# Optimization experiments

Hardware: AMD Instinct MI355X
Metric: run time of the kernel (lower is better)

The kernel has to match this reference:

```python
import jax, jax.numpy as jnp
from jax import lax
import numpy as np

THRESHOLD = 0.9
KHALF = 5  # conv_kernel_size; full conv width = 2*KHALF + 1 = 11


def _cif_scan(eouts, alpha_norm, elens, ylens, Lp1):
    """Vectorized-over-batch integrate-and-fire scan over time (lax.scan)."""
    B, T, D = eouts.shape
    bidx = jnp.arange(B)
    dt = eouts.dtype

    def step(carry, xs):
        alpha_accum, state, n_tok, fired = carry
        a_t, e_t, t = xs  # a_t: [B], e_t: [B,D], t: scalar int
        alpha_accum = alpha_accum + a_t
        active = (t <= elens - 1) & (n_tok < ylens)
        fire = active & (alpha_accum >= THRESHOLD)
        ak1 = 1.0 - alpha_accum
        ak2 = a_t - ak1
        # attention-weight column for time t
        aw_col = jnp.zeros((B, Lp1), dt)
        w_old = jnp.where(fire, ak1, jnp.where(active, a_t, jnp.zeros((), dt)))
        aw_col = aw_col.at[bidx, n_tok].add(w_old)
        n_new = n_tok + fire.astype(n_tok.dtype)
        aw_col = aw_col.at[bidx, n_new].add(jnp.where(fire, ak2, jnp.zeros((), dt)))
        # fired output row (set once per token slot)
        fire_val = state + ak1[:, None] * e_t
        cur = fired[bidx, n_tok]
        fired = fired.at[bidx, n_tok].set(jnp.where(fire[:, None], fire_val, cur))
        # integrate / reset state
        state = jnp.where(fire[:, None], ak2[:, None] * e_t,
                          jnp.where(active[:, None], state + a_t[:, None] * e_t, state))
        alpha_accum = jnp.where(fire, ak2, alpha_accum)
        return (alpha_accum, state, n_new, fired), aw_col

    init = (jnp.zeros((B,), dt), jnp.zeros((B, D), dt),
            jnp.zeros((B,), jnp.int32), jnp.zeros((B, Lp1, D), dt))
    xs = (jnp.swapaxes(alpha_norm, 0, 1), jnp.swapaxes(eouts, 0, 1),
          jnp.arange(T))
    (_, _, _, fired), aw_cols = lax.scan(step, init, xs)
    aws = jnp.transpose(aw_cols, (1, 2, 0))[:, None]  # [B,1,Lp1,T]
    return fired, aws


def _forward(eouts, conv_w, conv_b, proj_w, proj_b, elens, ylens, L):
    # Conv1d over time, 'same' padding: [B,T,D] -> [B,T,C]
    conv_feat = lax.conv_general_dilated(
        eouts, conv_w, window_strides=(1,), padding=[(KHALF, KHALF)],
        dimension_numbers=('NWC', 'WIO', 'NWC')) + conv_b
    alpha = jax.nn.sigmoid(conv_feat @ proj_w + proj_b)[:, :, 0]  # [B,T]
    alpha_norm = alpha / jnp.sum(alpha, axis=1, keepdims=True) \
        * ylens[:, None].astype(alpha.dtype)
    fired, aws = _cif_scan(eouts, alpha_norm, elens, ylens, L + 1)
    return fired[:, :L], alpha, aws


def setup_inputs():
    key = jax.random.key(0)
    k1, k2, k3, k4, k5 = jax.random.split(key, 5)
    B, T, D, C = 16, 2048, 512, 512
    eouts = jax.random.normal(k1, (B, T, D), jnp.float32)
    elens = jnp.maximum(jax.random.randint(k2, (B,), 0, T), T // 2).astype(jnp.int32)
    ylens = jnp.maximum(jax.random.randint(k3, (B,), 0, 128), 32).astype(jnp.int32)
    conv_w = jax.random.normal(k4, (2 * KHALF + 1, D, C), jnp.float32) * 0.02
    conv_b = jnp.zeros((C,), jnp.float32)
    proj_w = jax.random.normal(k5, (C, 1), jnp.float32) * 0.05
    proj_b = jnp.zeros((1,), jnp.float32)
    return dict(eouts=eouts, conv_w=conv_w, conv_b=conv_b,
                proj_w=proj_w, proj_b=proj_b, elens=elens, ylens=ylens)


def reference(eouts, conv_w, conv_b, proj_w, proj_b, elens, ylens):
    L = int(jnp.max(ylens))  # max_len = ylens.max(), as in the original
    return _forward(eouts, conv_w, conv_b, proj_w, proj_b, elens, ylens, L)
```

## Files before the change

### kernel.cpp

```cpp
#include <hip/hip_runtime.h>
#include <math.h>

#define KHALF 5
#define MAXF 256

__device__ inline float readlane_f(float v, int lane) {
    return __int_as_float(__builtin_amdgcn_readlane(__float_as_int(v), lane));
}

__global__ void k_prep(const float* __restrict__ conv_w, const float* __restrict__ conv_b,
                       const float* __restrict__ proj_w, const float* __restrict__ proj_b,
                       float* __restrict__ w_eff, float* __restrict__ b_eff,
                       int KD, int C,
                       float* __restrict__ aws, long long awsN, int WB, int NFILL) {
    if ((int)blockIdx.x >= WB) {
        long long N4 = awsN >> 2;
        long long gid = (long long)(blockIdx.x - WB) * 256 + threadIdx.x;
        float4 z = make_float4(0.f, 0.f, 0.f, 0.f);
        float4* a4 = reinterpret_cast<float4*>(aws);
        long long stride = (long long)NFILL * 256;
        for (long long i = gid; i < N4; i += stride) a4[i] = z;
        int tail = (int)(awsN & 3);
        if (gid < tail) aws[4 * N4 + gid] = 0.f;
        return;
    }
    int gid = blockIdx.x * blockDim.x + threadIdx.x;
    int wave = gid >> 6;
    int lane = gid & 63;
    if (wave > KD) return;
    float s = 0.f;
    if (wave < KD) {
        const float* row = conv_w + (size_t)wave * C;
        for (int c = lane * 4; c < C; c += 256) {
            float4 v = *reinterpret_cast<const float4*>(row + c);
            float4 w = *reinterpret_cast<const float4*>(proj_w + c);
            s += v.x * w.x + v.y * w.y + v.z * w.z + v.w * w.w;
        }
    } else {
        for (int c = lane; c < C; c += 64) s += conv_b[c] * proj_w[c];
    }
#pragma unroll
    for (int off = 32; off > 0; off >>= 1) s += __shfl_down(s, off, 64);
    if (lane == 0) {
        if (wave < KD) w_eff[wave] = s;
        else           b_eff[0] = s + proj_b[0];
    }
}

__global__ __launch_bounds__(256) void k_qdot(const float* __restrict__ eouts,
                                              const float* __restrict__ w_eff,
                                              float* __restrict__ q, int BT) {
    __shared__ float tile[64 * 68];
    __shared__ float wls[11 * 68];
    __shared__ float part[64 * 89];
    const int u0 = blockIdx.x * 64;
    const int rp = threadIdx.x & 31;
    const int s8 = threadIdx.x >> 5;
    float acc0[11], acc1[11];
#pragma unroll
    for (int k = 0; k < 11; ++k) { acc0[k] = 0.f; acc1[k] = 0.f; }

    float4 rv[4];
    float4 wv;
    auto issue = [&](int c) {
#pragma unroll
        for (int it = 0; it < 4; ++it) {
            int idx = it * 256 + threadIdx.x;
            int r = idx >> 4, j4 = idx & 15;
            rv[it] = *reinterpret_cast<const float4*>(
                eouts + (size_t)(u0 + r) * 512 + c * 64 + j4 * 4);
        }
        if (threadIdx.x < 176) {
            int k = threadIdx.x >> 4, sl = threadIdx.x & 15;
            wv = *reinterpret_cast<const float4*>(
                w_eff + k * 512 + c * 64 + sl * 4);
        }
    };
    issue(0);
    for (int c = 0; c < 8; ++c) {
        __syncthreads();
#pragma unroll
        for (int it = 0; it < 4; ++it) {
            int idx = it * 256 + threadIdx.x;
            int r = idx >> 4, j4 = idx & 15;
            *reinterpret_cast<float4*>(&tile[r * 68 + j4 * 4]) = rv[it];
        }
        if (threadIdx.x < 176) {
            int k = threadIdx.x >> 4, sl = threadIdx.x & 15;
            *reinterpret_cast<float4*>(&wls[k * 68 + sl * 4]) = wv;
        }
        __syncthreads();
        if (c + 1 < 8) issue(c + 1);
#pragma unroll
        for (int j4 = 0; j4 < 2; ++j4) {
            const int dl = s8 * 8 + j4 * 4;
            float4 a0 = *reinterpret_cast<const float4*>(&tile[rp * 68 + dl]);
            float4 a1 = *reinterpret_cast<const float4*>(&tile[(rp + 32) * 68 + dl]);
#pragma unroll
            for (int k = 0; k < 11; ++k) {
                float4 wvv = *reinterpret_cast<const float4*>(&wls[k * 68 + dl]);
                acc0[k] += a0.x * wvv.x + a0.y * wvv.y + a0.z * wvv.z + a0.w * wvv.w;
                acc1[k] += a1.x * wvv.x + a1.y * wvv.y + a1.z * wvv.z + a1.w * wvv.w;
            }
        }
    }
    __syncthreads();
#pragma unroll
    for (int k = 0; k < 11; ++k) {
        part[rp * 89 + s8 * 11 + k] = acc0[k];
        part[(rp + 32) * 89 + s8 * 11 + k] = acc1[k];
    }
    __syncthreads();
    if (threadIdx.x < 64) {
        int r = threadIdx.x;
        const float* p = &part[r * 89];
        float o[12];
#pragma unroll
        for (int k = 0; k < 11; ++k) {
            float s0 = (p[0 * 11 + k] + p[1 * 11 + k]) + (p[2 * 11 + k] + p[3 * 11 + k]);
            float s1 = (p[4 * 11 + k] + p[5 * 11 + k]) + (p[6 * 11 + k] + p[7 * 11 + k]);
            o[k] = s0 + s1;
        }
        o[11] = 0.f;
        float4* dst = reinterpret_cast<float4*>(q + (size_t)(u0 + r) * 12);
        dst[0] = make_float4(o[0], o[1], o[2], o[3]);
        dst[1] = make_float4(o[4], o[5], o[6], o[7]);
        dst[2] = make_float4(o[8], o[9], o[10], o[11]);
    }
}

__global__ __launch_bounds__(256) void k_sigpart(const float* __restrict__ q,
                                                 const float* __restrict__ b_eff,
                                                 float* __restrict__ alpha,
                                                 float* __restrict__ partials,
                                                 int T, int tcb,
                                                 float* __restrict__ aws,
                                                 long long awsN, int SB, int NFILL) {
    if ((int)blockIdx.x >= SB) {
        long long N4 = awsN >> 2;
        long long gid = (long long)(blockIdx.x - SB) * 256 + threadIdx.x;
        float4 z = make_float4(0.f, 0.f, 0.f, 0.f);
        float4* a4 = reinterpret_cast<float4*>(aws);
        long long stride = (long long)NFILL * 256;
        for (long long i = gid; i < N4; i += stride) a4[i] = z;
        int tail = (int)(awsN & 3);
        if (gid < tail) aws[4 * N4 + gid] = 0.f;
        return;
    }
    __shared__ float qs[266 * 12];
    __shared__ float psm[4];
    int bx = blockIdx.x;
    int b = bx / tcb, tc = bx % tcb;
    int t0 = tc * 256;
    const float* qb = q + (size_t)b * T * 12;
    const int base = (t0 - 5) * 12;
    const int lim = T * 12;
    for (int i = threadIdx.x; i < 266 * 12; i += 256) {
        int gi = base + i;
        qs[i] = (gi >= 0 && gi < lim) ? qb[gi] : 0.f;
    }
    __syncthreads();
    int t = t0 + threadIdx.x;
    float sacc = b_eff[0];
#pragma unroll
    for (int k = 0; k < 11; ++k) sacc += qs[(threadIdx.x + k) * 12 + k];
    float al = 1.f / (1.f + expf(-sacc));
    alpha[(size_t)b * T + t] = al;
    float s = al;
    int lane = threadIdx.x & 63;
    int w = threadIdx.x >> 6;
#pragma unroll
    for (int off = 32; off > 0; off >>= 1) s += __shfl_down(s, off, 64);
    if (lane == 0) psm[w] = s;
    __syncthreads();
    if (threadIdx.x == 0) {
        float tot = 0.f;
        for (int i = 0; i < 4; ++i) tot += psm[i];
        partials[bx] = tot;
    }
}

__global__ void k_alpha(const float* __restrict__ eouts,
                        const float* __restrict__ w_eff,
                        const float* __restrict__ b_eff,
                        float* __restrict__ alpha,
                        int B, int T, int D) {
    const int W = 2 * KHALF + 1;
    int gid = blockIdx.x * blockDim.x + threadIdx.x;
    int wave = gid >> 6;
    int lane = gid & 63;
    if (wave >= B * T) return;
    int b = wave / T;
    int t = wave - b * T;
    int WD = W * D;
    int t0 = t - KHALF;
    float s = 0.f;
    if (t0 >= 0 && t0 + W <= T) {
        const float* base = eouts + ((size_t)b * T + t0) * D;
        for (int j = lane * 4; j < WD; j += 256) {
            float4 v = *reinterpret_cast<const float4*>(base + j);
            float4 w = *reinterpret_cast<const float4*>(w_eff + j);
            s += v.x * w.x + v.y * w.y + v.z * w.z + v.w * w.w;
        }
    } else {
        const float* base = eouts + (size_t)b * T * D;
        for (int j = lane; j < WD; j += 64) {
            int tt = t0 + j / D;
            if (tt >= 0 && tt < T) {
                int d = j - (j / D) * D;
                s += base[(size_t)tt * D + d] * w_eff[j];
            }
        }
    }
#pragma unroll
    for (int off = 32; off > 0; off >>= 1) s += __shfl_down(s, off, 64);
    if (lane == 0) {
        float logit = s + b_eff[0];
        alpha[(size_t)b * T + t] = 1.f / (1.f + expf(-logit));
    }
}

__global__ void k_chain(const float* __restrict__ alpha_in,
                        int use_part,
                        const float* __restrict__ partials, int npart,
                        const int* __restrict__ elens,
                        const int* __restrict__ ylens,
                        float* __restrict__ anorm,
                        int* __restrict__ n_fired,
                        int* __restrict__ fire_t,
                        float* __restrict__ fire_a1,
                        float* __restrict__ fire_a2,
                        int T, int Lp1) {
    extern __shared__ float an[];
    float* pf = an + T;
    __shared__ float sm[16];
    __shared__ float stot;
    int b = blockIdx.x;
    const float* row = alpha_in + (size_t)b * T;
    if ((T & 1023) == 0) {
        const float4* r4 = reinterpret_cast<const float4*>(row);
        float4* a4 = reinterpret_cast<float4*>(an);
        for (int i = threadIdx.x; i < (T >> 2); i += blockDim.x) a4[i] = r4[i];
    } else {
        for (int i = threadIdx.x; i < T; i += blockDim.x) an[i] = row[i];
    }
    __syncthreads();
    if (use_part) {
        if (threadIdx.x < npart && threadIdx.x < 16)
            sm[threadIdx.x] = partials[b * npart + threadIdx.x];
        __syncthreads();
        if (threadIdx.x == 0) {
            float tot = 0.f;
            if (npart <= 16) { for (int i = 0; i < npart; ++i) tot += sm[i]; }
            else { for (int i = 0; i < npart; ++i) tot += partials[b * npart + i]; }
            stot = tot;
        }
    } else {
        float s = 0.f;
        for (int i = threadIdx.x; i < T; i += blockDim.x) s += an[i];
        int lane0 = threadIdx.x & 63;
        int w0 = threadIdx.x >> 6;
#pragma unroll
        for (int off = 32; off > 0; off >>= 1) s += __shfl_down(s, off, 64);
        if (lane0 == 0) sm[w0] = s;
        __syncthreads();
        if (threadIdx.x == 0) {
            float tot = 0.f;
            int nw = blockDim.x >> 6;
            for (int i = 0; i < nw; ++i) tot += sm[i];
            stot = tot;
        }
    }
    __syncthreads();
    float ssum = stot;
    float yl = (float)ylens[b];
    float* __restrict__ anb = anorm + (size_t)b * T;
    for (int i = threadIdx.x; i < T; i += blockDim.x) {
        float v = an[i] / ssum * yl;
        an[i] = v;
        anb[i] = v;
    }
    __syncthreads();
    {
        int wv = threadIdx.x >> 6, ln = threadIdx.x & 63;
        int nchunks = (T + 63) >> 6;
        for (int c = wv; c < nchunks; c += 4) {
            int t = c * 64 + ln;
            float P = (t < T) ? an[t] : 0.f;
#pragma unroll
            for (int off = 1; off < 64; off <<= 1) {
                float tmp = __shfl_up(P, off, 64);
                if (ln >= off) P += tmp;
            }
            if (t < T) pf[t] = P;
        }
    }
    __syncthreads();
    if (threadIdx.x >= 64) return;
    int lane = threadIdx.x;
    int elen = elens[b];
    if (elen > T) elen = T;
    const int ylen = ylens[b];
    int* __restrict__ ft = fire_t + (size_t)b * Lp1;
    float* __restrict__ fa1 = fire_a1 + (size_t)b * Lp1;
    float* __restrict__ fa2 = fire_a2 + (size_t)b * Lp1;
    float accum = 0.f;
    int n = 0;
    bool done = false;
    for (int t0 = 0; t0 < elen && !done; t0 += 64) {
        int nv = elen - t0;
        if (nv > 64) nv = 64;
        bool inb = (t0 + lane < T);
        float P = inb ? pf[t0 + lane] : 0.f;
        float av = inb ? an[t0 + lane] : 0.f;
        unsigned long long validmask = (nv == 64) ? ~0ull : ((1ull << nv) - 1ull);
        float base = accum;
        int start = 0;
        while (true) {
            bool cond = (base + P >= 0.9f);
            unsigned long long bal = __ballot(cond) & validmask;
            if (start > 0) bal &= (~0ull) << start;
            if (bal == 0) break;
            int u = __builtin_ctzll(bal);
            float Pu = readlane_f(P, u);
            float au = readlane_f(av, u);
            float accum_f = base + Pu;
            float ak1 = 1.f - accum_f;
            float ak2 = au - ak1;
            if (lane == 0) { ft[n] = t0 + u; fa1[n] = ak1; fa2[n] = ak2; }
            ++n;
            if (n >= ylen) { done = true; break; }
            base = ak2 - Pu;
            start = u + 1;
            if (start >= nv) break;
        }
        if (!done) accum = base + readlane_f(P, nv - 1);
    }
    if (lane == 0) n_fired[b] = n;
}

__global__ void k_awfired(const float* __restrict__ eouts,
                          const float* __restrict__ anorm,
                          const int* __restrict__ elens,
                          const int* __restrict__ ylens,
                          const int* __restrict__ n_fired,
                          const int* __restrict__ fire_t,
                          const float* __restrict__ fire_a1,
                          const float* __restrict__ fire_a2,
                          float* __restrict__ aws,
                          float* __restrict__ fired,
                          int T, int D, int L, int Lp1,
                          int AB, int tcpb) {
    if ((int)blockIdx.x < AB) {
        __shared__ int fts[MAXF];
        __shared__ float a1s[MAXF];
        __shared__ float a2s[MAXF];
        int b = blockIdx.x / tcpb;
        int tc = blockIdx.x % tcpb;
        int nf = n_fired[b];
        for (int i = threadIdx.x; i < nf; i += blockDim.x) {
            fts[i] = fire_t[(size_t)b * Lp1 + i];
            a1s[i] = fire_a1[(size_t)b * Lp1 + i];
            a2s[i] = fire_a2[(size_t)b * Lp1 + i];
        }
        __syncthreads();
        int t = tc * 256 + threadIdx.x;
        if (t >= T) return;
        int elen = elens[b];
        if (elen > T) elen = T;
        int ylen = ylens[b];
        if (t >= elen) return;
        int lo = 0, hi = nf;
        while (lo < hi) {
            int mid = (lo + hi) >> 1;
            if (fts[mid] < t) lo = mid + 1; else hi = mid;
        }
        int rowi = lo;
        bool isfire = (rowi < nf && fts[rowi] == t);
        float* col = aws + (size_t)b * Lp1 * T + t;
        if (isfire) {
            col[(size_t)rowi * T] = a1s[rowi];
            col[(size_t)(rowi + 1) * T] = a2s[rowi];
        } else if (rowi < ylen) {
            col[(size_t)rowi * T] = anorm[(size_t)b * T + t];
        }
    } else {
        __shared__ float4 red[128];
        int idx = blockIdx.x - AB;
        int b = idx / L;
        int n = idx % L;
        int h = threadIdx.x >> 7;
        int dl = threadIdx.x & 127;
        int nf = n_fired[b];
        if ((D & 3) == 0) {
            int D4 = D >> 2;
            float4* dst = reinterpret_cast<float4*>(fired + ((size_t)b * L + n) * D);
            if (n >= nf) {
                if (h == 0) {
                    for (int d4 = dl; d4 < D4; d4 += 128)
                        dst[d4] = make_float4(0.f, 0.f, 0.f, 0.f);
                }
                return;
            }
            int t0 = (n == 0) ? 0 : fire_t[(size_t)b * Lp1 + n - 1];
            int t1 = fire_t[(size_t)b * Lp1 + n];
            float ak1 = fire_a1[(size_t)b * Lp1 + n];
            float ak2p = (n > 0) ? fire_a2[(size_t)b * Lp1 + n - 1] : 0.f;
            const float* an_g = anorm + (size_t)b * T;
            const float4* E = reinterpret_cast<const float4*>(eouts + (size_t)b * T * D);
            for (int d0 = 0; d0 < D4; d0 += 128) {
                int d4 = d0 + dl;
                float4 acc = make_float4(0.f, 0.f, 0.f, 0.f);
                if (d4 < D4) {
                    float4 a0 = acc, a1 = acc, a2 = acc, a3 = acc;
                    int t = t0 + h;
                    for (; t + 6 <= t1; t += 8) {
                        float w0 = (t == t1) ? ak1 : ((t == t0 && n > 0) ? ak2p : an_g[t]);
                        float w1 = (t + 2 == t1) ? ak1 : an_g[t + 2];
                        float w2 = (t + 4 == t1) ? ak1 : an_g[t + 4];
                        float w3 = (t + 6 == t1) ? ak1 : an_g[t + 6];
                        float4 v0 = E[(size_t)t * D4 + d4];
                        float4 v1 = E[(size_t)(t + 2) * D4 + d4];
                        float4 v2 = E[(size_t)(t + 4) * D4 + d4];
                        float4 v3 = E[(size_t)(t + 6) * D4 + d4];
                        a0.x += w0 * v0.x; a0.y += w0 * v0.y; a0.z += w0 * v0.z; a0.w += w0 * v0.w;
                        a1.x += w1 * v1.x; a1.y += w1 * v1.y; a1.z += w1 * v1.z; a1.w += w1 * v1.w;
                        a2.x += w2 * v2.x; a2.y += w2 * v2.y; a2.z += w2 * v2.z; a2.w += w2 * v2.w;
                        a3.x += w3 * v3.x; a3.y += w3 * v3.y; a3.z += w3 * v3.z; a3.w += w3 * v3.w;
                    }
                    for (; t <= t1; t += 2) {
                        float wt = (t == t1) ? ak1 : ((t == t0 && n > 0) ? ak2p : an_g[t]);
                        float4 v = E[(size_t)t * D4 + d4];
                        a0.x += wt * v.x; a0.y += wt * v.y; a0.z += wt * v.z; a0.w += wt * v.w;
                    }
                    acc.x = (a0.x + a1.x) + (a2.x + a3.x);
                    acc.y = (a0.y + a1.y) + (a2.y + a3.y);
                    acc.z = (a0.z + a1.z) + (a2.z + a3.z);
                    acc.w = (a0.w + a1.w) + (a2.w + a3.w);
                }
                if (h == 1 && d4 < D4) red[dl] = acc;
                __syncthreads();
                if (h == 0 && d4 < D4) {
                    float4 o = red[dl];
                    acc.x += o.x; acc.y += o.y; acc.z += o.z; acc.w += o.w;
                    dst[d4] = acc;
                }
                __syncthreads();
            }
        } else {
            float* dst = fired + ((size_t)b * L + n) * D;
            if (n >= nf) {
                for (int d = threadIdx.x; d < D; d += 256) dst[d] = 0.f;
                return;
            }
            int t0 = (n == 0) ? 0 : fire_t[(size_t)b * Lp1 + n - 1];
            int t1 = fire_t[(size_t)b * Lp1 + n];
            float ak1 = fire_a1[(size_t)b * Lp1 + n];
            float ak2p = (n > 0) ? fire_a2[(size_t)b * Lp1 + n - 1] : 0.f;
            const float* an_g = anorm + (size_t)b * T;
            for (int d = threadIdx.x; d < D; d += 256) {
                const float* e = eouts + ((size_t)b * T + t0) * D + d;
                float accv;
                if (t1 == t0) {
                    accv = ak1 * e[0];
                } else {
                    float w0 = (n > 0) ? ak2p : an_g[t0];
                    accv = w0 * e[0];
                    float a0 = 0.f, a1 = 0.f, a2 = 0.f, a3 = 0.f;
                    int t = t0 + 1;
                    const float* ee = e + D;
                    for (; t + 3 < t1; t += 4, ee += 4 * (size_t)D) {
                        a0 += an_g[t]     * ee[0];
                        a1 += an_g[t + 1] * ee[D];
                        a2 += an_g[t + 2] * ee[2 * (size_t)D];
                        a3 += an_g[t + 3] * ee[3 * (size_t)D];
                    }
                    for (; t < t1; ++t, ee += D) a0 += an_g[t] * ee[0];
                    accv += ((a0 + a1) + (a2 + a3));
                    accv += ak1 * ee[0];
                }
                dst[d] = accv;
            }
        }
    }
}

extern "C" void kernel_launch(void* const* d_in, const int* in_sizes, int n_in,
                              void* d_out, int out_size, void* d_ws, size_t ws_size,
                              hipStream_t stream) {
    const float* eouts  = (const float*)d_in[0];
    const float* conv_w = (const float*)d_in[1];
    const float* conv_b = (const float*)d_in[2];
    const float* proj_w = (const float*)d_in[3];
    const float* proj_b = (const float*)d_in[4];
    const int*   elens  = (const int*)d_in[5];
    const int*   ylens  = (const int*)d_in[6];

    const int B = in_sizes[5];
    const int C = in_sizes[2];
    const int W = 2 * KHALF + 1;
    const int D = in_sizes[1] / (W * C);
    const int T = in_sizes[0] / (B * D);
    const int L = (out_size - 2 * B * T) / (B * (D + T));
    const int Lp1 = L + 1;
    const int BT = B * T;
    const int tcb = (T + 255) / 256;

    float* out   = (float*)d_out;
    float* fired = out;
    float* alpha = out + (size_t)B * L * D;
    float* aws   = alpha + (size_t)B * T;

    char*  ws        = (char*)d_ws;
    float* w_eff     = (float*)ws;
    float* b_eff     = (float*)(ws + (size_t)W * D * 4);
    int*   n_fired   = (int*)(b_eff + 16);
    int*   fire_t    = n_fired + B + 16;
    float* fire_a1   = (float*)(fire_t + (size_t)B * Lp1 + 16);
    float* fire_a2   = fire_a1 + (size_t)B * Lp1 + 16;
    float* anorm     = fire_a2 + (size_t)B * Lp1 + 16;
    float* qbuf      = anorm + (size_t)B * T + 16;
    float* partials  = qbuf + (size_t)BT * 12 + 16;
    size_t ws_need   = (size_t)((char*)(partials + (size_t)B * tcb + 16) - ws);

    const int KD = W * D;
    const long long awsN = (long long)B * Lp1 * T;
    long long wthreads = (long long)(KD + 1) * 64;
    int WB = (int)((wthreads + 255) / 256);
    const int NFILL = 2048;

    const bool fast = (ws_size >= ws_need) && (D == 512) && (C == 512) &&
                      (BT % 64 == 0) && (T % 256 == 0) && (T <= 16384) &&
                      (Lp1 <= MAXF);

    if (fast) {
        k_prep<<<WB, 256, 0, stream>>>(conv_w, conv_b, proj_w, proj_b,
                                       w_eff, b_eff, KD, C,
                                       aws, awsN, WB, 0);
        k_qdot<<<BT / 64, 256, 0, stream>>>(eouts, w_eff, qbuf, BT);
        int SB = B * tcb;
        k_sigpart<<<SB + NFILL, 256, 0, stream>>>(qbuf, b_eff, alpha, partials,
                                                  T, tcb, aws, awsN, SB, NFILL);
    } else {
        k_prep<<<WB + NFILL, 256, 0, stream>>>(conv_w, conv_b, proj_w, proj_b,
                                               w_eff, b_eff, KD, C,
                                               aws, awsN, WB, NFILL);
        long long threads = (long long)BT * 64;
        int blocks = (int)((threads + 255) / 256);
        k_alpha<<<blocks, 256, 0, stream>>>(eouts, w_eff, b_eff, alpha, B, T, D);
    }

    k_chain<<<B, 256, 2 * T * sizeof(float), stream>>>(
        alpha, fast ? 1 : 0, partials, tcb,
        elens, ylens, anorm,
        n_fired, fire_t, fire_a1, fire_a2, T, Lp1);

    {
        int tcpb = (T + 255) / 256;
        int AB = B * tcpb;
        int FB = B * L;
        k_awfired<<<AB + FB, 256, 0, stream>>>(eouts, anorm,
                                               elens, ylens, n_fired,
                                               fire_t, fire_a1, fire_a2,
                                               aws, fired, T, D, L, Lp1,
                                               AB, tcpb);
    }
}
```

Before: 172.7 us.

## Move aws zero-fill to prep kernel, drop qdot prefetch, split fired sum contiguously

```diff
diff --git a/kernel.cpp b/kernel.cpp
--- a/kernel.cpp
+++ b/kernel.cpp
@@ -59,38 +59,23 @@
     float acc0[11], acc1[11];
 #pragma unroll
     for (int k = 0; k < 11; ++k) { acc0[k] = 0.f; acc1[k] = 0.f; }
-
-    float4 rv[4];
-    float4 wv;
-    auto issue = [&](int c) {
+    for (int c = 0; c < 8; ++c) {
+        __syncthreads();
 #pragma unroll
         for (int it = 0; it < 4; ++it) {
             int idx = it * 256 + threadIdx.x;
             int r = idx >> 4, j4 = idx & 15;
-            rv[it] = *reinterpret_cast<const float4*>(
+            float4 v = *reinterpret_cast<const float4*>(
                 eouts + (size_t)(u0 + r) * 512 + c * 64 + j4 * 4);
+            *reinterpret_cast<float4*>(&tile[r * 68 + j4 * 4]) = v;
         }
         if (threadIdx.x < 176) {
             int k = threadIdx.x >> 4, sl = threadIdx.x & 15;
-            wv = *reinterpret_cast<const float4*>(
+            float4 wv = *reinterpret_cast<const float4*>(
                 w_eff + k * 512 + c * 64 + sl * 4);
-        }
-    };
-    issue(0);
-    for (int c = 0; c < 8; ++c) {
+            *reinterpret_cast<float4*>(&wls[k * 68 + sl * 4]) = wv;
+        }
         __syncthreads();
-#pragma unroll
-        for (int it = 0; it < 4; ++it) {
-            int idx = it * 256 + threadIdx.x;
-            int r = idx >> 4, j4 = idx & 15;
-            *reinterpret_cast<float4*>(&tile[r * 68 + j4 * 4]) = rv[it];
-        }
-        if (threadIdx.x < 176) {
-            int k = threadIdx.x >> 4, sl = threadIdx.x & 15;
-            *reinterpret_cast<float4*>(&wls[k * 68 + sl * 4]) = wv;
-        }
-        __syncthreads();
-        if (c + 1 < 8) issue(c + 1);
 #pragma unroll
         for (int j4 = 0; j4 < 2; ++j4) {
             const int dl = s8 * 8 + j4 * 4;
@@ -98,9 +83,9 @@
             float4 a1 = *reinterpret_cast<const float4*>(&tile[(rp + 32) * 68 + dl]);
 #pragma unroll
             for (int k = 0; k < 11; ++k) {
-                float4 wvv = *reinterpret_cast<const float4*>(&wls[k * 68 + dl]);
-                acc0[k] += a0.x * wvv.x + a0.y * wvv.y + a0.z * wvv.z + a0.w * wvv.w;
-                acc1[k] += a1.x * wvv.x + a1.y * wvv.y + a1.z * wvv.z + a1.w * wvv.w;
+                float4 wv = *reinterpret_cast<const float4*>(&wls[k * 68 + dl]);
+                acc0[k] += a0.x * wv.x + a0.y * wv.y + a0.z * wv.z + a0.w * wv.w;
+                acc1[k] += a1.x * wv.x + a1.y * wv.y + a1.z * wv.z + a1.w * wv.w;
             }
         }
     }
@@ -133,20 +118,7 @@
                                                  const float* __restrict__ b_eff,
                                                  float* __restrict__ alpha,
                                                  float* __restrict__ partials,
-                                                 int T, int tcb,
-                                                 float* __restrict__ aws,
-                                                 long long awsN, int SB, int NFILL) {
-    if ((int)blockIdx.x >= SB) {
-        long long N4 = awsN >> 2;
-        long long gid = (long long)(blockIdx.x - SB) * 256 + threadIdx.x;
-        float4 z = make_float4(0.f, 0.f, 0.f, 0.f);
-        float4* a4 = reinterpret_cast<float4*>(aws);
-        long long stride = (long long)NFILL * 256;
-        for (long long i = gid; i < N4; i += stride) a4[i] = z;
-        int tail = (int)(awsN & 3);
-        if (gid < tail) aws[4 * N4 + gid] = 0.f;
-        return;
-    }
+                                                 int T, int tcb) {
     __shared__ float qs[266 * 12];
     __shared__ float psm[4];
     int bx = blockIdx.x;
@@ -407,30 +379,33 @@
             float ak1 = fire_a1[(size_t)b * Lp1 + n];
             float ak2p = (n > 0) ? fire_a2[(size_t)b * Lp1 + n - 1] : 0.f;
             const float* an_g = anorm + (size_t)b * T;
-            const float4* E = reinterpret_cast<const float4*>(eouts + (size_t)b * T * D);
+            float wfirst = (n > 0) ? ak2p : an_g[t0];
+            int len = t1 - t0 + 1;
+            int half0 = len >> 1;
+            int ts = h ? (t0 + half0) : t0;
+            int te = h ? t1 : (t0 + half0 - 1);
+            const float4* Eb = reinterpret_cast<const float4*>(eouts + (size_t)b * T * D);
             for (int d0 = 0; d0 < D4; d0 += 128) {
                 int d4 = d0 + dl;
                 float4 acc = make_float4(0.f, 0.f, 0.f, 0.f);
-                if (d4 < D4) {
+                if (d4 < D4 && ts <= te) {
                     float4 a0 = acc, a1 = acc, a2 = acc, a3 = acc;
-                    int t = t0 + h;
-                    for (; t + 6 <= t1; t += 8) {
-                        float w0 = (t == t1) ? ak1 : ((t == t0 && n > 0) ? ak2p : an_g[t]);
-                        float w1 = (t + 2 == t1) ? ak1 : an_g[t + 2];
-                        float w2 = (t + 4 == t1) ? ak1 : an_g[t + 4];
-                        float w3 = (t + 6 == t1) ? ak1 : an_g[t + 6];
-                        float4 v0 = E[(size_t)t * D4 + d4];
-                        float4 v1 = E[(size_t)(t + 2) * D4 + d4];
-                        float4 v2 = E[(size_t)(t + 4) * D4 + d4];
-                        float4 v3 = E[(size_t)(t + 6) * D4 + d4];
-                        a0.x += w0 * v0.x; a0.y += w0 * v0.y; a0.z += w0 * v0.z; a0.w += w0 * v0.w;
-                        a1.x += w1 * v1.x; a1.y += w1 * v1.y; a1.z += w1 * v1.z; a1.w += w1 * v1.w;
-                        a2.x += w2 * v2.x; a2.y += w2 * v2.y; a2.z += w2 * v2.z; a2.w += w2 * v2.w;
-                        a3.x += w3 * v3.x; a3.y += w3 * v3.y; a3.z += w3 * v3.z; a3.w += w3 * v3.w;
+                    int t = ts;
+                    const float4* ee = Eb + (size_t)ts * D4 + d4;
+                    for (; t + 3 <= te; t += 4, ee += 4 * (size_t)D4) {
+                        float w0 = (t == t1)     ? ak1 : ((t == t0)     ? wfirst : an_g[t]);
+                        float w1 = (t + 1 == t1) ? ak1 : an_g[t + 1];
+                        float w2 = (t + 2 == t1) ? ak1 : an_g[t + 2];
+                        float w3 = (t + 3 == t1) ? ak1 : an_g[t + 3];
+                        float4 va = ee[0], vb = ee[D4], vc = ee[2 * (size_t)D4], vd = ee[3 * (size_t)D4];
+                        a0.x += w0 * va.x; a0.y += w0 * va.y; a0.z += w0 * va.z; a0.w += w0 * va.w;
+                        a1.x += w1 * vb.x; a1.y += w1 * vb.y; a1.z += w1 * vb.z; a1.w += w1 * vb.w;
+                        a2.x += w2 * vc.x; a2.y += w2 * vc.y; a2.z += w2 * vc.z; a2.w += w2 * vc.w;
+                        a3.x += w3 * vd.x; a3.y += w3 * vd.y; a3.z += w3 * vd.z; a3.w += w3 * vd.w;
                     }
-                    for (; t <= t1; t += 2) {
-                        float wt = (t == t1) ? ak1 : ((t == t0 && n > 0) ? ak2p : an_g[t]);
-                        float4 v = E[(size_t)t * D4 + d4];
+                    for (; t <= te; ++t, ee += D4) {
+                        float wt = (t == t1) ? ak1 : ((t == t0) ? wfirst : an_g[t]);
+                        float4 v = ee[0];
                         a0.x += wt * v.x; a0.y += wt * v.y; a0.z += wt * v.z; a0.w += wt * v.w;
                     }
                     acc.x = (a0.x + a1.x) + (a2.x + a3.x);
@@ -524,27 +499,23 @@
     size_t ws_need   = (size_t)((char*)(partials + (size_t)B * tcb + 16) - ws);
 
     const int KD = W * D;
-    const long long awsN = (long long)B * Lp1 * T;
-    long long wthreads = (long long)(KD + 1) * 64;
-    int WB = (int)((wthreads + 255) / 256);
-    const int NFILL = 2048;
+    {
+        long long wthreads = (long long)(KD + 1) * 64;
+        int WB = (int)((wthreads + 255) / 256);
+        int NFILL = 2048;
+        long long awsN = (long long)B * Lp1 * T;
+        k_prep<<<WB + NFILL, 256, 0, stream>>>(conv_w, conv_b, proj_w, proj_b,
+                                               w_eff, b_eff, KD, C,
+                                               aws, awsN, WB, NFILL);
+    }
 
     const bool fast = (ws_size >= ws_need) && (D == 512) && (C == 512) &&
                       (BT % 64 == 0) && (T % 256 == 0) && (T <= 16384) &&
                       (Lp1 <= MAXF);
-
     if (fast) {
-        k_prep<<<WB, 256, 0, stream>>>(conv_w, conv_b, proj_w, proj_b,
-                                       w_eff, b_eff, KD, C,
-                                       aws, awsN, WB, 0);
         k_qdot<<<BT / 64, 256, 0, stream>>>(eouts, w_eff, qbuf, BT);
-        int SB = B * tcb;
-        k_sigpart<<<SB + NFILL, 256, 0, stream>>>(qbuf, b_eff, alpha, partials,
-                                                  T, tcb, aws, awsN, SB, NFILL);
+        k_sigpart<<<B * tcb, 256, 0, stream>>>(qbuf, b_eff, alpha, partials, T, tcb);
     } else {
-        k_prep<<<WB + NFILL, 256, 0, stream>>>(conv_w, conv_b, proj_w, proj_b,
-                                               w_eff, b_eff, KD, C,
-                                               aws, awsN, WB, NFILL);
         long long threads = (long long)BT * 64;
         int blocks = (int)((threads + 255) / 256);
         k_alpha<<<blocks, 256, 0, stream>>>(eouts, w_eff, b_eff, alpha, B, T, D);
```

Result: faster. 160.8 us (-6.9%).
